# Kernel tuning notes

Hardware: AMD Instinct MI355X
Metric: run time of the kernel (lower is better)

The kernel has to match this reference:

```python
import jax, jax.numpy as jnp
import numpy as np

EPS = 1e-08
KERNEL = 3


def setup_inputs() -> dict:
    key = jax.random.key(0)
    k1, k2, k3, k4 = jax.random.split(key, 4)
    N, IN_CH, OUT_CH, H, W, STYLE_DIM = 16, 256, 256, 64, 64, 512
    x = jax.random.normal(k1, (N, IN_CH, H, W), dtype=jnp.float32)
    style = jax.random.normal(k2, (N, STYLE_DIM), dtype=jnp.float32)
    # base weight: [1, out_ch, in_ch, k, k] (torch.randn init)
    weight = jax.random.normal(k3, (1, OUT_CH, IN_CH, KERNEL, KERNEL), dtype=jnp.float32)
    # modulation Linear(style_dim -> in_ch): weight ~ N(0,1), bias = 0
    mod_w = jax.random.normal(k4, (IN_CH, STYLE_DIM), dtype=jnp.float32)
    mod_b = jnp.zeros((IN_CH,), dtype=jnp.float32)
    return {"x": x, "style": style, "weight": weight, "mod_w": mod_w, "mod_b": mod_b}


def _per_sample_conv(xi, wi):
    # xi: [in_ch, H, W], wi: [out_ch, in_ch, k, k]
    pad = KERNEL // 2
    out = jax.lax.conv_general_dilated(
        xi[None], wi,
        window_strides=(1, 1),
        padding=[(pad, pad), (pad, pad)],
        dimension_numbers=("NCHW", "OIHW", "NCHW"),
    )
    return out[0]  # [out_ch, H, W]


def reference(x, style, weight, mod_w, mod_b):
    # modulation: Linear(style) -> [N, in_ch]
    s = style @ mod_w.T + mod_b  # [N, in_ch]
    # modulate base weight: [N, out_ch, in_ch, k, k]
    w = weight * (s[:, None, :, None, None] + 1.0)
    # demodulate
    demod = jax.lax.rsqrt(jnp.sum(w * w, axis=(2, 3, 4)) + EPS)  # [N, out_ch]
    w = w * demod[:, :, None, None, None]
    # grouped conv with groups=N == per-sample conv, vmapped over batch
    out = jax.vmap(_per_sample_conv)(x, w)  # [N, out_ch, H, W]
    return out
```

## Files before the change

### kernel.cpp

```cpp
#include <hip/hip_runtime.h>
#include <hip/hip_bf16.h>
#include <stdint.h>


#define NB  16
#define IC  256
#define OC  256
#define HW  64
#define HWP 66
#define SD  512
#define SPATIAL 4096
#define HWPIC 16896

typedef __hip_bfloat16 bf16;
typedef __bf16 bf16x8 __attribute__((ext_vector_type(8)));
typedef float  f32x4  __attribute__((ext_vector_type(4)));
typedef uint32_t u32a3 __attribute__((address_space(3)));
typedef const uint32_t u32a1 __attribute__((address_space(1)));

static __device__ __forceinline__ unsigned short f2bu(float f) {
    bf16 h = __float2bfloat16(f);
    union { bf16 b; unsigned short u; } c; c.b = h; return c.u;
}
static __device__ __forceinline__ void gll16(const void* g, void* l) {
    __builtin_amdgcn_global_load_lds((u32a1*)g, (u32a3*)l, 16, 0, 0);
}

__global__ __launch_bounds__(256)
void k_prep1(const float* __restrict__ weight, const float* __restrict__ style,
             const float* __restrict__ mod_w, const float* __restrict__ mod_b,
             float* __restrict__ wsq, bf16* __restrict__ wt2,
             uint4* __restrict__ xs4, float* __restrict__ scale) {
    int b = blockIdx.x, t = threadIdx.x;
    if (b < 256) {
        int tid = b * 256 + t;
        const float* wp = weight + (size_t)tid * 9;
        float v[9], s = 0.f;
        #pragma unroll
        for (int r = 0; r < 9; ++r) { v[r] = wp[r]; s += v[r] * v[r]; }
        wsq[tid] = s;
        #pragma unroll
        for (int r = 0; r < 9; ++r) wt2[(r << 16) + tid] = __float2bfloat16(v[r]);
    } else if (b < 784) {
        int idx = b - 256;
        int n = idx / 33, bx = idx - n * 33;
        int f = bx * 256 + t;
        int u = f >> 5, q = f & 31;
        if (u >= 260) return;
        int rb;
        if      (u <  66) rb = u;
        else if (u < 132) rb = 65 * 66 + (u - 66);
        else if (u < 196) rb = (u - 131) * 66;
        else              rb = (u - 195) * 66 + 65;
        xs4[(size_t)n * 139392 + rb * 32 + q] = make_uint4(0u, 0u, 0u, 0u);
    } else {
        int lane = t & 63;
        int w = (b - 784) * 4 + (t >> 6);
        int n = w >> 8, ic = w & 255;
        const float4* mw4 = (const float4*)mod_w + (size_t)ic * 128 + lane * 2;
        const float4* st4 = (const float4*)style + (size_t)n * 128 + lane * 2;
        float4 a0 = mw4[0], a1 = mw4[1], s0 = st4[0], s1 = st4[1];
        float acc = a0.x*s0.x + a0.y*s0.y + a0.z*s0.z + a0.w*s0.w
                  + a1.x*s1.x + a1.y*s1.y + a1.z*s1.z + a1.w*s1.w;
        #pragma unroll
        for (int off = 32; off > 0; off >>= 1) acc += __shfl_down(acc, off);
        if (lane == 0) scale[w] = acc + mod_b[ic] + 1.0f;
    }
}

__global__ __launch_bounds__(256)
void k_prep2(const float* __restrict__ x, const float* __restrict__ scale,
             const float* __restrict__ wsq, bf16* __restrict__ xs,
             float* __restrict__ demod) {
    __shared__ unsigned short tile[HW * 256];
    int b = blockIdx.x, t = threadIdx.x;
    if (b < 1024) {
        int y = b & 63, n = b >> 6;
        const float* sc = scale + n * IC;
        const float4* xp4 = (const float4*)(x + ((size_t)n * IC) * SPATIAL + (size_t)y * HW);
        #pragma unroll
        for (int i = 0; i < 16; ++i) {
            int fid = i * 256 + t;
            int ic = fid >> 4, f4 = fid & 15;
            float4 v = xp4[(size_t)ic * 1024 + f4];
            float s = sc[ic];
            int sp = f4 << 2;
            int sw = ic ^ ((f4 & 7) << 3);
            tile[(sp + 0) * 256 + sw] = f2bu(v.x * s);
            tile[(sp + 1) * 256 + sw] = f2bu(v.y * s);
            tile[(sp + 2) * 256 + sw] = f2bu(v.z * s);
            tile[(sp + 3) * 256 + sw] = f2bu(v.w * s);
        }
        __syncthreads();
        uint4* dst4 = (uint4*)(xs + (((size_t)n * HWP + (y + 1)) * HWP + 1) * IC);
        #pragma unroll
        for (int j = 0; j < 8; ++j) {
            int uid = j * 256 + t;
            int sp = uid >> 5, g = uid & 31;
            dst4[sp * 32 + g] =
                *(const uint4*)&tile[sp * 256 + ((g ^ ((sp >> 2) & 7)) << 3)];
        }
    } else {
        int n = b - 1024, oc = t;
        float* sc = (float*)tile;
        sc[t] = scale[n * IC + t];
        __syncthreads();
        const float4* wp4 = (const float4*)(wsq + (size_t)oc * IC);
        const float4* sc4 = (const float4*)sc;
        float acc = 0.f;
        #pragma unroll 8
        for (int i = 0; i < 64; ++i) {
            float4 q = wp4[i], s = sc4[i];
            acc += q.x*s.x*s.x + q.y*s.y*s.y + q.z*s.z*s.z + q.w*s.w*s.w;
        }
        demod[n * OC + oc] = rsqrtf(acc + 1e-8f);
    }
}

#define VM4 asm volatile("s_waitcnt vmcnt(4)" ::: "memory")
#define VM2 asm volatile("s_waitcnt vmcnt(2)" ::: "memory")
#define VM0 asm volatile("s_waitcnt vmcnt(0)" ::: "memory")
#define BAR __builtin_amdgcn_s_barrier()

__global__ __launch_bounds__(512, 2)
void k_conv(const bf16* __restrict__ xs, const bf16* __restrict__ wt2,
            const float* __restrict__ demod, float* __restrict__ out) {
    extern __shared__ char smem[];
    int t = threadIdx.x, l = t & 63, w = t >> 6;
    int wm = w & 1, wn = w >> 1;
    int bid = blockIdx.x;
    int work = ((bid & 7) << 5) | (bid >> 3);
    int nimg = work >> 4;
    int ybase = (work & 15) << 2;
    int spb = (work & 15) << 8;

    int srow = (w << 3) + (l >> 3);
    int gseg = (l & 7) ^ (l >> 3);
    const bf16* gA = xs + (((size_t)nimg * HWP + ybase) * HWP + srow) * IC + (gseg << 3);
    const bf16* gB = wt2 + ((size_t)srow << 8) + (gseg << 3);
    int stW = w << 10;

    int aRow = ((wm << 6) + (l & 15)) << 7;
    int bRow = ((wn << 5) + (l & 15)) << 7;
    int sg0 = ((l >> 4) ^ (l & 7)) << 4;
    int sg1 = sg0 ^ 64;

    f32x4 acc[4][4][2];
    #pragma unroll
    for (int p = 0; p < 4; ++p)
        #pragma unroll
        for (int m = 0; m < 4; ++m)
            #pragma unroll
            for (int n = 0; n < 2; ++n) acc[p][m][n] = (f32x4){0.f, 0.f, 0.f, 0.f};

    bf16x8 af[4][2], bf0[2][2], bf1[2][2];

#define STG_A(ha, PARN, AOFF) do {                                          \
    const bf16* s_ = gA + (AOFF) + (ha) * 2 * HWPIC;                        \
    char* d_ = smem + (PARN) * 32768 + (ha) * 16384 + stW;                  \
    gll16(s_, d_); gll16(s_ + HWPIC, d_ + 8192); } while (0)
#define STG_B(hb, PARN, BOFF) do {                                          \
    const bf16* s_ = gB + (BOFF) + (hb) * (128 * IC);                       \
    char* d_ = smem + 65536 + (PARN) * 32768 + (hb) * 16384 + stW;          \
    gll16(s_, d_); gll16(s_ + 64 * IC, d_ + 8192); } while (0)
#define LD_A(QA) do { const char* Ab_ = Ap + (QA) * 16384 + aRow;           \
    _Pragma("unroll") for (int m_ = 0; m_ < 4; ++m_) {                      \
        af[m_][0] = *(const bf16x8*)(Ab_ + m_ * 2048 + sg0);                \
        af[m_][1] = *(const bf16x8*)(Ab_ + m_ * 2048 + sg1); } } while (0)
#define LD_B(DST, QB) do { const char* Bb_ = Bp + (QB) * 16384 + bRow;      \
    _Pragma("unroll") for (int n_ = 0; n_ < 2; ++n_) {                      \
        DST[n_][0] = *(const bf16x8*)(Bb_ + n_ * 2048 + sg0);               \
        DST[n_][1] = *(const bf16x8*)(Bb_ + n_ * 2048 + sg1); } } while (0)
#define MM(P, BF) do {                                                      \
    __builtin_amdgcn_s_setprio(1);                                          \
    _Pragma("unroll") for (int kk_ = 0; kk_ < 2; ++kk_)                     \
    _Pragma("unroll") for (int m_ = 0; m_ < 4; ++m_)                        \
    _Pragma("unroll") for (int n_ = 0; n_ < 2; ++n_)                        \
        acc[P][m_][n_] = __builtin_amdgcn_mfma_f32_16x16x32_bf16(           \
            af[m_][kk_], BF[n_][kk_], acc[P][m_][n_], 0, 0, 0);             \
    __builtin_amdgcn_s_setprio(0); } while (0)

    STG_A(0, 0, 0);
    STG_B(0, 0, 0);
    STG_B(1, 0, 0);
    STG_A(1, 0, 0);
    VM4;
    BAR;

    #pragma clang loop unroll(disable)
    for (int T = 0; T < 35; ++T) {
        int par = T & 1, parn = par ^ 1;
        const char* Ap = smem + par * 32768;
        const char* Bp = smem + 65536 + par * 32768;
        int Tn = T + 1;
        int rn = Tn >> 2, icn = (Tn & 3) << 6;
        int kyn = rn / 3, kxn = rn - kyn * 3;
        int aoffN = (kyn * HWP + kxn) * IC + icn;
        int boffN = (rn << 16) + icn;

        LD_A(0); LD_B(bf0, 0);
        STG_A(0, parn, aoffN);
        VM4; BAR; MM(0, bf0);
        LD_B(bf1, 1);
        STG_B(0, parn, boffN);
        VM4; BAR; MM(1, bf1);
        LD_A(1);
        STG_B(1, parn, boffN);
        BAR; MM(2, bf1);
        STG_A(1, parn, aoffN);
        VM4; BAR; MM(3, bf0);
    }
    {
        const char* Ap = smem + 32768;
        const char* Bp = smem + 65536 + 32768;
        LD_A(0); LD_B(bf0, 0);
        VM2; BAR; MM(0, bf0);
        LD_B(bf1, 1);
        VM0; BAR; MM(1, bf1);
        LD_A(1);
        MM(2, bf1);
        MM(3, bf0);
    }

    const float* dm = demod + nimg * OC;
    int ocol = l & 15, orow = (l >> 4) << 2;
    #pragma unroll
    for (int p = 0; p < 4; ++p) {
        int qa = p >> 1, qb = qa ^ (p & 1);
        #pragma unroll
        for (int n = 0; n < 2; ++n) {
            int oc = (qb << 7) + (wn << 5) + (n << 4) + ocol;
            float d = dm[oc];
            size_t ob = ((size_t)(nimg * OC + oc)) * SPATIAL
                      + spb + (qa << 7) + (wm << 6) + orow;
            #pragma unroll
            for (int m = 0; m < 4; ++m) {
                f32x4 a = acc[p][m][n];
                f32x4 o = { a[0] * d, a[1] * d, a[2] * d, a[3] * d };
                *reinterpret_cast<f32x4*>(out + ob + m * 16) = o;
            }
        }
    }
}

extern "C" void kernel_launch(void* const* d_in, const int* in_sizes, int n_in,
                              void* d_out, int out_size, void* d_ws, size_t ws_size,
                              hipStream_t stream) {
    const float* x      = (const float*)d_in[0];
    const float* style  = (const float*)d_in[1];
    const float* weight = (const float*)d_in[2];
    const float* mod_w  = (const float*)d_in[3];
    const float* mod_b  = (const float*)d_in[4];
    float* out = (float*)d_out;

    char* ws = (char*)d_ws;
    float* scale = (float*)(ws + 0);
    float* demod = (float*)(ws + 16384);
    float* wsq   = (float*)(ws + 32768);
    bf16*  wt2   = (bf16*)(ws + 294912);
    bf16*  xs    = (bf16*)(ws + 1474560);

    static int s_attr = 0;
    if (!s_attr) {
        hipFuncSetAttribute(reinterpret_cast<const void*>(k_conv),
                            hipFuncAttributeMaxDynamicSharedMemorySize, 131072);
        s_attr = 1;
    }

    k_prep1<<<1808, 256, 0, stream>>>(weight, style, mod_w, mod_b,
                                      wsq, wt2, (uint4*)xs, scale);
    k_prep2<<<1040, 256, 0, stream>>>(x, scale, wsq, xs, demod);
    k_conv<<<256, 512, 131072, stream>>>(xs, wt2, demod, out);
}
```

Before: 186.2 us.

## Deepen conv prefetch pipeline by issuing A half-tile loads two steps ahead

```diff
diff --git a/kernel.cpp b/kernel.cpp
--- a/kernel.cpp
+++ b/kernel.cpp
@@ -117,9 +117,7 @@
     }
 }
 
-#define VM4 asm volatile("s_waitcnt vmcnt(4)" ::: "memory")
-#define VM2 asm volatile("s_waitcnt vmcnt(2)" ::: "memory")
-#define VM0 asm volatile("s_waitcnt vmcnt(0)" ::: "memory")
+#define VM6 asm volatile("s_waitcnt vmcnt(6)" ::: "memory")
 #define BAR __builtin_amdgcn_s_barrier()
 
 __global__ __launch_bounds__(512, 2)
@@ -184,42 +182,35 @@
     STG_B(0, 0, 0);
     STG_B(1, 0, 0);
     STG_A(1, 0, 0);
-    VM4;
+    STG_A(0, 1, 64);
+    VM6;
     BAR;
 
     #pragma clang loop unroll(disable)
-    for (int T = 0; T < 35; ++T) {
+    for (int T = 0; T < 36; ++T) {
         int par = T & 1, parn = par ^ 1;
         const char* Ap = smem + par * 32768;
         const char* Bp = smem + 65536 + par * 32768;
-        int Tn = T + 1;
-        int rn = Tn >> 2, icn = (Tn & 3) << 6;
-        int kyn = rn / 3, kxn = rn - kyn * 3;
-        int aoffN = (kyn * HWP + kxn) * IC + icn;
-        int boffN = (rn << 16) + icn;
+        int T1 = T + 1, T2 = T + 2;
+        int r1 = T1 >> 2, ic1 = (T1 & 3) << 6;
+        int ky1 = r1 / 3, kx1 = r1 - ky1 * 3;
+        int aoff1 = T1 < 36 ? (ky1 * HWP + kx1) * IC + ic1 : 0;
+        int boff1 = T1 < 36 ? (r1 << 16) + ic1 : 0;
+        int r2 = T2 >> 2, ic2 = (T2 & 3) << 6;
+        int ky2 = r2 / 3, kx2 = r2 - ky2 * 3;
+        int aoff2 = T2 < 36 ? (ky2 * HWP + kx2) * IC + ic2 : 0;
 
         LD_A(0); LD_B(bf0, 0);
-        STG_A(0, parn, aoffN);
-        VM4; BAR; MM(0, bf0);
+        STG_B(0, parn, boff1);
+        VM6; BAR; MM(0, bf0);
         LD_B(bf1, 1);
-        STG_B(0, parn, boffN);
-        VM4; BAR; MM(1, bf1);
+        STG_B(1, parn, boff1);
+        VM6; BAR; MM(1, bf1);
         LD_A(1);
-        STG_B(1, parn, boffN);
+        STG_A(1, parn, aoff1);
         BAR; MM(2, bf1);
-        STG_A(1, parn, aoffN);
-        VM4; BAR; MM(3, bf0);
-    }
-    {
-        const char* Ap = smem + 32768;
-        const char* Bp = smem + 65536 + 32768;
-        LD_A(0); LD_B(bf0, 0);
-        VM2; BAR; MM(0, bf0);
-        LD_B(bf1, 1);
-        VM0; BAR; MM(1, bf1);
-        LD_A(1);
-        MM(2, bf1);
-        MM(3, bf0);
+        STG_A(0, par, aoff2);
+        VM6; BAR; MM(3, bf0);
     }
 
     const float* dm = demod + nimg * OC;
```

Result: no change. 189.1 us (+1.6%).
